# Kernel tuning notes

Measured on AMD Instinct MI355X. Metric: run time of the kernel, lower is better.

The kernel has to match this reference:

```python
import jax, jax.numpy as jnp
import numpy as np
from jax import lax

BETA = 0.95     # snn.Leaky(0.95)
THRESH = 1.0    # snntorch default threshold
ALPHA = 2.0     # snntorch ATan surrogate default alpha
NUM_STEPS = 100

@jax.custom_vjp
def spike_fn(u):
    return (u > 0).astype(u.dtype)

def _spike_fwd(u):
    return (u > 0).astype(u.dtype), u

def _spike_bwd(u, g):
    surr = (ALPHA / 2.0) / (1.0 + (jnp.pi / 2.0 * ALPHA * u) ** 2)
    return (g * surr,)

spike_fn.defvjp(_spike_fwd, _spike_bwd)

def leaky_scan(inputs, mem0):
    # inputs: [T, ...]; snntorch Leaky with reset_mechanism='zero'
    def step(carry, x_t):
        mem, _ = carry
        reset = spike_fn(mem - THRESH)       # spike detected from previous mem
        base = BETA * mem + x_t
        mem = base - reset * base            # zero-reset
        spk = spike_fn(mem - THRESH)
        return (mem, spk), None
    (mem, spk), _ = lax.scan(step, (mem0, jnp.zeros_like(mem0)), inputs)
    return spk, mem

def setup_inputs():
    key = jax.random.key(0)
    ks = jax.random.split(key, 7)
    B, T, W, C = 32, 2000, 512, 4
    H, O = 1024, 10
    s = lambda n: 1.0 / np.sqrt(n)
    return {
        "x": jax.random.normal(ks[0], (B, T, W, C), jnp.float32),
        "conv_w": jax.random.uniform(ks[1], (C,), jnp.float32, -s(C), s(C)),
        "conv_b": jax.random.uniform(ks[2], (), jnp.float32, -s(C), s(C)),
        "hidden_w": jax.random.uniform(ks[3], (H, W), jnp.float32, -s(W), s(W)),
        "hidden_b": jax.random.uniform(ks[4], (H,), jnp.float32, -s(W), s(W)),
        "out_w": jax.random.uniform(ks[5], (O, H), jnp.float32, -s(H), s(H)),
        "out_b": jax.random.uniform(ks[6], (O,), jnp.float32, -s(H), s(H)),
    }

def reference(x, conv_w, conv_b, hidden_w, hidden_b, out_w, out_b):
    B, T, W, _ = x.shape
    # 1x1 conv fusing 4 antenna channels: (B,T,W,4)->(B,T,W)
    fused = jnp.einsum('bhwc,c->bhw', x, conv_w) + conv_b
    G = T // NUM_STEPS
    fused = fused.reshape(B, G, NUM_STEPS, W)      # [B,G,S,W]
    seq1 = jnp.moveaxis(fused, 2, 0)               # [S,B,G,W] time-major
    spk, _ = leaky_scan(seq1, jnp.zeros((B, G, W), x.dtype))
    hidden = spk @ hidden_w.T + hidden_b           # [B,G,H]
    seq2 = jnp.moveaxis(hidden, 1, 0)              # [G,B,H]
    spk2, _ = leaky_scan(seq2, jnp.zeros((B, hidden.shape[2]), x.dtype))
    out = spk2 @ out_w.T + out_b                   # [B,O]
    return jax.nn.softmax(out, axis=1)
```

## Files before the change

### kernel.cpp

```cpp
#include <hip/hip_runtime.h>
#include <hip/hip_bf16.h>

typedef float f32x4 __attribute__((ext_vector_type(4)));

#define NB 32
#define NT 2000
#define NW 512
#define NG 20
#define NS 100
#define NH 1024
#define NO 10
#define BETA 0.95f
#define THRESH 1.0f

__global__ __launch_bounds__(256) void k1_conv_scan_tr(
    const f32x4* __restrict__ x,
    const float* __restrict__ cw,
    const float* __restrict__ cb,
    float* __restrict__ spk1,
    const float* __restrict__ wsrc,
    float* __restrict__ wT,
    int* __restrict__ counter)
{
    __shared__ float tile[32][33];
    int bid = blockIdx.x;

    if (bid < 1280) {
        int half = bid & 1;
        int bg = bid >> 1;
        int g = bg % NG;
        int b = bg / NG;
        int tid = threadIdx.x;

        const f32x4* __restrict__ base =
            x + ((size_t)(b * NT + g * NS) * NW + half * 256);

        float w0 = cw[0], w1 = cw[1], w2 = cw[2], w3 = cw[3];
        float bias = cb[0];

        f32x4 A[10], B[10];
        float mem = 0.0f;

#define LOAD10(dst, S0)                                                        \
    {                                                                          \
        _Pragma("unroll")                                                      \
        for (int j = 0; j < 10; ++j)                                           \
            dst[j] = __builtin_nontemporal_load(base + (tid + ((S0) + j) * NW)); \
    }
#define STEP10(src)                                                            \
    {                                                                          \
        _Pragma("unroll")                                                      \
        for (int j = 0; j < 10; ++j) {                                         \
            f32x4 v = src[j];                                                  \
            float f = fmaf(v[0], w0, fmaf(v[1], w1,                            \
                      fmaf(v[2], w2, fmaf(v[3], w3, bias))));                  \
            float base_m = fmaf(BETA, mem, f);                                 \
            mem = (mem > THRESH) ? 0.0f : base_m;                              \
        }                                                                      \
    }

        LOAD10(A, 0)
        LOAD10(B, 10) STEP10(A)
        LOAD10(A, 20) STEP10(B)
        LOAD10(B, 30) STEP10(A)
        LOAD10(A, 40) STEP10(B)
        LOAD10(B, 50) STEP10(A)
        LOAD10(A, 60) STEP10(B)
        LOAD10(B, 70) STEP10(A)
        LOAD10(A, 80) STEP10(B)
        LOAD10(B, 90) STEP10(A)
        STEP10(B)
#undef LOAD10
#undef STEP10

        spk1[(b * NG + g) * NW + half * 256 + tid] = (mem > THRESH) ? 1.0f : 0.0f;
    } else {
        int tbid = bid - 1280;
        if (tbid == 0 && threadIdx.x == 0) *counter = 0;
        int bk = tbid & 15;
        int bh = tbid >> 4;
        int tx = threadIdx.x & 31;
        int ty = threadIdx.x >> 5;
        #pragma unroll
        for (int j = 0; j < 4; ++j)
            tile[ty + j * 8][tx] = wsrc[(bh * 32 + ty + j * 8) * NW + bk * 32 + tx];
        __syncthreads();
        #pragma unroll
        for (int j = 0; j < 4; ++j)
            wT[(bk * 32 + ty + j * 8) * NH + bh * 32 + tx] = tile[tx][ty + j * 8];
    }
}

__global__ __launch_bounds__(256) void k2_hidden_scan(
    const float* __restrict__ spk1,
    const float* __restrict__ wT,
    const float* __restrict__ hb,
    const float* __restrict__ ow,
    const float* __restrict__ ob,
    float* __restrict__ partial,
    int* __restrict__ counter,
    float* __restrict__ out)
{
    __shared__ __align__(16) char smem[40960];
    float (*sk)[NW]     = (float (*)[NW])smem;
    f32x4 (*red)[NG][16] = (f32x4 (*)[NG][16])smem;
    __shared__ int lastFlag;

    int bid = blockIdx.x;
    int b = bid >> 4;
    int hgrp = bid & 15;
    int t = threadIdx.x;
    int lane4 = t & 15;
    int c = t >> 4;
    int h = hgrp * 64 + lane4 * 4;

    {
        const f32x4* __restrict__ sp4 =
            (const f32x4*)(spk1 + (size_t)b * NG * NW);
        f32x4* sk4 = (f32x4*)smem;
        #pragma unroll
        for (int i = 0; i < 10; ++i)
            sk4[t + i * 256] = sp4[t + i * 256];
    }
    __syncthreads();

    f32x4 acc[NG];
    #pragma unroll
    for (int g = 0; g < NG; ++g)
        #pragma unroll
        for (int j = 0; j < 4; ++j) acc[g][j] = 0.0f;

    int k0 = c * 32;
    #pragma unroll
    for (int kkg = 0; kkg < 8; ++kkg) {
        int kk = k0 + (((kkg + c) & 7) << 2);
        f32x4 w0 = *(const f32x4*)&wT[(kk + 0) * NH + h];
        f32x4 w1 = *(const f32x4*)&wT[(kk + 1) * NH + h];
        f32x4 w2 = *(const f32x4*)&wT[(kk + 2) * NH + h];
        f32x4 w3 = *(const f32x4*)&wT[(kk + 3) * NH + h];
        #pragma unroll
        for (int g = 0; g < NG; ++g) {
            f32x4 u = *(const f32x4*)&sk[g][kk];
            #pragma unroll
            for (int j = 0; j < 4; ++j)
                acc[g][j] = fmaf(u[0], w0[j], fmaf(u[1], w1[j],
                            fmaf(u[2], w2[j], fmaf(u[3], w3[j], acc[g][j]))));
        }
    }

    __syncthreads();
    if (c < 8) {
        #pragma unroll
        for (int g = 0; g < NG; ++g) red[c][g][lane4] = acc[g];
    }
    __syncthreads();
    if (c >= 8) {
        #pragma unroll
        for (int g = 0; g < NG; ++g) {
            f32x4 v = red[c - 8][g][lane4];
            #pragma unroll
            for (int j = 0; j < 4; ++j) v[j] += acc[g][j];
            red[c - 8][g][lane4] = v;
        }
    }
    __syncthreads();

    if (t < 64) {
        float hbias = hb[hgrp * 64 + t];
        int hl = t >> 2, hj = t & 3;
        float mem = 0.0f;
        #pragma unroll
        for (int g = 0; g < NG; ++g) {
            float xin = hbias;
            #pragma unroll
            for (int cc = 0; cc < 8; ++cc) xin += red[cc][g][hl][hj];
            float base = fmaf(BETA, mem, xin);
            mem = (mem > THRESH) ? 0.0f : base;
        }
        float spike = (mem > THRESH) ? 1.0f : 0.0f;

        #pragma unroll
        for (int o = 0; o < NO; ++o) {
            float p = spike * ow[o * NH + hgrp * 64 + t];
            p += __shfl_down(p, 32);
            p += __shfl_down(p, 16);
            p += __shfl_down(p, 8);
            p += __shfl_down(p, 4);
            p += __shfl_down(p, 2);
            p += __shfl_down(p, 1);
            if (t == 0) partial[(b * 16 + hgrp) * NO + o] = p;
        }
    }

    if (t == 0) {
        __threadfence();
        int old = atomicAdd(counter, 1);
        lastFlag = (old == NB * 16 - 1);
    }
    __syncthreads();
    if (lastFlag) {
        __threadfence();
        if (t < NB) {
            const float* p = partial + t * 16 * NO;
            float v[NO];
            #pragma unroll
            for (int o = 0; o < NO; ++o) v[o] = ob[o];
            #pragma unroll
            for (int hg = 0; hg < 16; ++hg)
                #pragma unroll
                for (int o = 0; o < NO; ++o) v[o] += p[hg * NO + o];

            float mx = -1e30f;
            #pragma unroll
            for (int o = 0; o < NO; ++o) mx = fmaxf(mx, v[o]);
            float sum = 0.0f;
            #pragma unroll
            for (int o = 0; o < NO; ++o) { v[o] = expf(v[o] - mx); sum += v[o]; }
            float inv = 1.0f / sum;
            #pragma unroll
            for (int o = 0; o < NO; ++o) out[t * NO + o] = v[o] * inv;
        }
    }
}

extern "C" void kernel_launch(void* const* d_in, const int* in_sizes, int n_in,
                              void* d_out, int out_size, void* d_ws, size_t ws_size,
                              hipStream_t stream) {
    const f32x4*  x  = (const f32x4*)d_in[0];
    const float*  cw = (const float*)d_in[1];
    const float*  cb = (const float*)d_in[2];
    const float*  hw = (const float*)d_in[3];
    const float*  hb = (const float*)d_in[4];
    const float*  ow = (const float*)d_in[5];
    const float*  ob = (const float*)d_in[6];
    float* out = (float*)d_out;

    char* ws = (char*)d_ws;
    float* spk1    = (float*)(ws);
    float* wT      = (float*)(ws + 1310720);
    float* partial = (float*)(ws + 1310720 + 2097152);
    int*   counter = (int*)(ws + 1310720 + 2097152 + 20480);

    k1_conv_scan_tr<<<1792, 256, 0, stream>>>(x, cw, cb, spk1, hw, wT, counter);

    k2_hidden_scan<<<NB * 16, 256, 0, stream>>>(spk1, wT, hb, ow, ob,
                                                partial, counter, out);
}
```

Before: 110.4 us.

## Widen hidden-layer blocks to 512 threads and move softmax to separate kernel

The hidden-layer kernel now runs 256 blocks of 512 threads, each covering 128 hidden units instead of 64, with a two-pass, two-level shared-memory reduction over the K-split. The last-block atomic counter and threadfence path is removed, and the final bias-plus-softmax runs in a small third kernel. The aim is fewer blocks, more reuse of the staged spikes per block, and no global atomics, at the cost of an extra launch and more reduction barriers. The K-loop is only partially unrolled and its bank-conflict skew is dropped, which could raise LDS conflicts or stalls.

```diff
diff --git a/kernel.cpp b/kernel.cpp
--- a/kernel.cpp
+++ b/kernel.cpp
@@ -19,8 +19,7 @@
     const float* __restrict__ cb,
     float* __restrict__ spk1,
     const float* __restrict__ wsrc,
-    float* __restrict__ wT,
-    int* __restrict__ counter)
+    float* __restrict__ wT)
 {
     __shared__ float tile[32][33];
     int bid = blockIdx.x;
@@ -76,7 +75,6 @@
         spk1[(b * NG + g) * NW + half * 256 + tid] = (mem > THRESH) ? 1.0f : 0.0f;
     } else {
         int tbid = bid - 1280;
-        if (tbid == 0 && threadIdx.x == 0) *counter = 0;
         int bk = tbid & 15;
         int bh = tbid >> 4;
         int tx = threadIdx.x & 31;
@@ -91,36 +89,32 @@
     }
 }
 
-__global__ __launch_bounds__(256) void k2_hidden_scan(
+__global__ __launch_bounds__(512, 2) void k2_hidden_scan(
     const float* __restrict__ spk1,
     const float* __restrict__ wT,
     const float* __restrict__ hb,
     const float* __restrict__ ow,
-    const float* __restrict__ ob,
-    float* __restrict__ partial,
-    int* __restrict__ counter,
-    float* __restrict__ out)
+    float* __restrict__ partial)
 {
     __shared__ __align__(16) char smem[40960];
-    float (*sk)[NW]     = (float (*)[NW])smem;
-    f32x4 (*red)[NG][16] = (f32x4 (*)[NG][16])smem;
-    __shared__ int lastFlag;
+    float (*sk)[NW] = (float (*)[NW])smem;
+    f32x4 (*red)[10][32] = (f32x4 (*)[10][32])smem;
 
     int bid = blockIdx.x;
-    int b = bid >> 4;
-    int hgrp = bid & 15;
+    int b = bid >> 3;
+    int hgrp = bid & 7;
     int t = threadIdx.x;
-    int lane4 = t & 15;
-    int c = t >> 4;
-    int h = hgrp * 64 + lane4 * 4;
+    int lane5 = t & 31;
+    int c = t >> 5;
+    int h = hgrp * 128 + lane5 * 4;
 
     {
         const f32x4* __restrict__ sp4 =
             (const f32x4*)(spk1 + (size_t)b * NG * NW);
         f32x4* sk4 = (f32x4*)smem;
         #pragma unroll
-        for (int i = 0; i < 10; ++i)
-            sk4[t + i * 256] = sp4[t + i * 256];
+        for (int i = 0; i < 5; ++i)
+            sk4[t + i * 512] = sp4[t + i * 512];
     }
     __syncthreads();
 
@@ -131,9 +125,9 @@
         for (int j = 0; j < 4; ++j) acc[g][j] = 0.0f;
 
     int k0 = c * 32;
-    #pragma unroll
+    #pragma unroll 2
     for (int kkg = 0; kkg < 8; ++kkg) {
-        int kk = k0 + (((kkg + c) & 7) << 2);
+        int kk = k0 + kkg * 4;
         f32x4 w0 = *(const f32x4*)&wT[(kk + 0) * NH + h];
         f32x4 w1 = *(const f32x4*)&wT[(kk + 1) * NH + h];
         f32x4 w2 = *(const f32x4*)&wT[(kk + 2) * NH + h];
@@ -148,78 +142,94 @@
         }
     }
 
-    __syncthreads();
-    if (c < 8) {
-        #pragma unroll
-        for (int g = 0; g < NG; ++g) red[c][g][lane4] = acc[g];
-    }
-    __syncthreads();
-    if (c >= 8) {
-        #pragma unroll
-        for (int g = 0; g < NG; ++g) {
-            f32x4 v = red[c - 8][g][lane4];
-            #pragma unroll
-            for (int j = 0; j < 4; ++j) v[j] += acc[g][j];
-            red[c - 8][g][lane4] = v;
-        }
-    }
-    __syncthreads();
-
-    if (t < 64) {
-        float hbias = hb[hgrp * 64 + t];
-        int hl = t >> 2, hj = t & 3;
-        float mem = 0.0f;
-        #pragma unroll
-        for (int g = 0; g < NG; ++g) {
-            float xin = hbias;
-            #pragma unroll
-            for (int cc = 0; cc < 8; ++cc) xin += red[cc][g][hl][hj];
-            float base = fmaf(BETA, mem, xin);
-            mem = (mem > THRESH) ? 0.0f : base;
-        }
+    float hbias = 0.0f, mem = 0.0f;
+    if (t < 128) hbias = hb[hgrp * 128 + t];
+    int hl = t >> 2, hj = t & 3;
+
+    #pragma unroll
+    for (int pass = 0; pass < 2; ++pass) {
+        __syncthreads();
+        if (c < 8) {
+            #pragma unroll
+            for (int gg = 0; gg < 10; ++gg)
+                red[c][gg][lane5] = acc[pass * 10 + gg];
+        }
+        __syncthreads();
+        if (c >= 8) {
+            #pragma unroll
+            for (int gg = 0; gg < 10; ++gg) {
+                f32x4 v = red[c - 8][gg][lane5];
+                f32x4 a = acc[pass * 10 + gg];
+                #pragma unroll
+                for (int j = 0; j < 4; ++j) v[j] += a[j];
+                red[c - 8][gg][lane5] = v;
+            }
+        }
+        __syncthreads();
+        if (c >= 4 && c < 8) {
+            #pragma unroll
+            for (int gg = 0; gg < 10; ++gg) {
+                f32x4 v = red[c - 4][gg][lane5];
+                f32x4 a = red[c][gg][lane5];
+                #pragma unroll
+                for (int j = 0; j < 4; ++j) v[j] += a[j];
+                red[c - 4][gg][lane5] = v;
+            }
+        }
+        __syncthreads();
+        if (t < 128) {
+            #pragma unroll
+            for (int gg = 0; gg < 10; ++gg) {
+                float xin = red[0][gg][hl][hj] + red[1][gg][hl][hj]
+                          + red[2][gg][hl][hj] + red[3][gg][hl][hj] + hbias;
+                float base = fmaf(BETA, mem, xin);
+                mem = (mem > THRESH) ? 0.0f : base;
+            }
+        }
+    }
+
+    if (t < 128) {
         float spike = (mem > THRESH) ? 1.0f : 0.0f;
-
+        int slot = hgrp * 2 + (t >> 6);
         #pragma unroll
         for (int o = 0; o < NO; ++o) {
-            float p = spike * ow[o * NH + hgrp * 64 + t];
+            float p = spike * ow[o * NH + hgrp * 128 + t];
             p += __shfl_down(p, 32);
             p += __shfl_down(p, 16);
             p += __shfl_down(p, 8);
             p += __shfl_down(p, 4);
             p += __shfl_down(p, 2);
             p += __shfl_down(p, 1);
-            if (t == 0) partial[(b * 16 + hgrp) * NO + o] = p;
-        }
-    }
-
-    if (t == 0) {
-        __threadfence();
-        int old = atomicAdd(counter, 1);
-        lastFlag = (old == NB * 16 - 1);
-    }
-    __syncthreads();
-    if (lastFlag) {
-        __threadfence();
-        if (t < NB) {
-            const float* p = partial + t * 16 * NO;
-            float v[NO];
-            #pragma unroll
-            for (int o = 0; o < NO; ++o) v[o] = ob[o];
-            #pragma unroll
-            for (int hg = 0; hg < 16; ++hg)
-                #pragma unroll
-                for (int o = 0; o < NO; ++o) v[o] += p[hg * NO + o];
-
-            float mx = -1e30f;
-            #pragma unroll
-            for (int o = 0; o < NO; ++o) mx = fmaxf(mx, v[o]);
-            float sum = 0.0f;
-            #pragma unroll
-            for (int o = 0; o < NO; ++o) { v[o] = expf(v[o] - mx); sum += v[o]; }
-            float inv = 1.0f / sum;
-            #pragma unroll
-            for (int o = 0; o < NO; ++o) out[t * NO + o] = v[o] * inv;
-        }
+            if ((t & 63) == 0) partial[(b * 16 + slot) * NO + o] = p;
+        }
+    }
+}
+
+__global__ __launch_bounds__(64) void k_softmax(
+    const float* __restrict__ partial,
+    const float* __restrict__ ob,
+    float* __restrict__ out)
+{
+    int t = threadIdx.x;
+    if (t < NB) {
+        const float* p = partial + t * 16 * NO;
+        float v[NO];
+        #pragma unroll
+        for (int o = 0; o < NO; ++o) v[o] = ob[o];
+        #pragma unroll
+        for (int hg = 0; hg < 16; ++hg)
+            #pragma unroll
+            for (int o = 0; o < NO; ++o) v[o] += p[hg * NO + o];
+
+        float mx = -1e30f;
+        #pragma unroll
+        for (int o = 0; o < NO; ++o) mx = fmaxf(mx, v[o]);
+        float sum = 0.0f;
+        #pragma unroll
+        for (int o = 0; o < NO; ++o) { v[o] = expf(v[o] - mx); sum += v[o]; }
+        float inv = 1.0f / sum;
+        #pragma unroll
+        for (int o = 0; o < NO; ++o) out[t * NO + o] = v[o] * inv;
     }
 }
 
@@ -239,10 +249,10 @@
     float* spk1    = (float*)(ws);
     float* wT      = (float*)(ws + 1310720);
     float* partial = (float*)(ws + 1310720 + 2097152);
-    int*   counter = (int*)(ws + 1310720 + 2097152 + 20480);
-
-    k1_conv_scan_tr<<<1792, 256, 0, stream>>>(x, cw, cb, spk1, hw, wT, counter);
-
-    k2_hidden_scan<<<NB * 16, 256, 0, stream>>>(spk1, wT, hb, ow, ob,
-                                                partial, counter, out);
-}
+
+    k1_conv_scan_tr<<<1792, 256, 0, stream>>>(x, cw, cb, spk1, hw, wT);
+
+    k2_hidden_scan<<<NB * 8, 512, 0, stream>>>(spk1, wT, hb, ow, partial);
+
+    k_softmax<<<1, 64, 0, stream>>>(partial, ob, out);
+}
```

New measurement: 105.4 us. 4.6% less time.
